# Kernel tuning notes

Hardware: AMD Instinct MI355X
Metric: run time of the kernel (lower is better)

Reference implementation:

```python
import jax, jax.numpy as jnp
import numpy as np

IN_FEATURES_LS = (32, 64, 128, 256)
OUT_FEATURES = 1024
B, T = 16, 4096


def setup_inputs() -> dict:
    key = jax.random.key(0)
    k_x, k_idx, k_w, k_b = jax.random.split(key, 4)
    n = len(IN_FEATURES_LS)
    x = jax.random.normal(k_x, (B, T, OUT_FEATURES), dtype=jnp.float32)
    # per-row declared feature size, drawn from the configured list
    branch_idx = jax.random.randint(k_idx, (B, T), 0, n)
    in_feat_size = jnp.array(IN_FEATURES_LS, dtype=jnp.int32)[branch_idx]
    # kaiming_uniform_(a=sqrt(5)) on (n, out, out): fan_in = out, bound = 1/sqrt(fan_in)
    bound_w = 1.0 / np.sqrt(OUT_FEATURES)
    weight = jax.random.uniform(k_w, (n, OUT_FEATURES, OUT_FEATURES), dtype=jnp.float32,
                                minval=-bound_w, maxval=bound_w)
    bound_b = 1.0 / np.sqrt(OUT_FEATURES)
    bias = jax.random.uniform(k_b, (n, OUT_FEATURES), dtype=jnp.float32,
                              minval=-bound_b, maxval=bound_b)
    return {"x": x, "in_feat_size": in_feat_size, "weight": weight, "bias": bias}


def reference(x, in_feat_size, weight, bias):
    # Loop over the small fixed set of feature-size branches (matches original).
    out = jnp.zeros(x.shape[:-1] + (OUT_FEATURES,), dtype=x.dtype)
    for idx, feat_size in enumerate(IN_FEATURES_LS):
        mask = (in_feat_size == feat_size)[..., None].astype(x.dtype)  # [B,T,1]
        y = jnp.einsum('oi,bti->bto', weight[idx], x) + bias[idx]
        out = out + mask * y
    return out
```

## Files before the change

### kernel.cpp

```cpp
#include <hip/hip_runtime.h>
#include <hip/hip_bf16.h>

#define OUTF 1024
#define NROWS 65536
#define NBR 4
#define BM 128
#define BN 256
#define BK 64
#define KITERS 16
#define ABYTES 16384
#define BBYTES 32768
#define BUFB 49152
#define NWG 2064

typedef __attribute__((ext_vector_type(8))) short short8;
typedef __attribute__((ext_vector_type(4))) float f32x4;

__device__ inline unsigned short f2bf(float f) {
    return __builtin_bit_cast(unsigned short, (__bf16)f);
}
__device__ inline void gload_lds16(const void* g, void* l) {
    __builtin_amdgcn_global_load_lds(
        (const __attribute__((address_space(1))) void*)g,
        (__attribute__((address_space(3))) void*)l, 16, 0, 0);
}
__device__ inline short8 pack8(float4 a, float4 b) {
    short8 o;
    o[0] = (short)f2bf(a.x); o[1] = (short)f2bf(a.y);
    o[2] = (short)f2bf(a.z); o[3] = (short)f2bf(a.w);
    o[4] = (short)f2bf(b.x); o[5] = (short)f2bf(b.y);
    o[6] = (short)f2bf(b.z); o[7] = (short)f2bf(b.w);
    return o;
}

__global__ void k_count(const int* __restrict__ feat, int* __restrict__ cnt) {
    __shared__ int lc[NBR];
    int tid = threadIdx.x;
    if (tid < NBR) lc[tid] = 0;
    __syncthreads();
    int r = blockIdx.x * 256 + tid;
    int b = 26 - __clz(feat[r]);
    atomicAdd(&lc[b], 1);
    __syncthreads();
    if (tid < NBR && lc[tid]) atomicAdd(&cnt[tid], lc[tid]);
}

__global__ void k_prefix(int* __restrict__ ws) {
    if (threadIdx.x == 0) {
        int s = 0;
        for (int b = 0; b < NBR; b++) { ws[4 + b] = s; s += ws[b]; ws[8 + b] = 0; }
    }
}

__global__ void k_fill(const int* __restrict__ feat, int* __restrict__ ws,
                       int* __restrict__ rowlist) {
    int tid = threadIdx.x;
    int lane = tid & 63;
    int r = blockIdx.x * 256 + tid;
    int b = 26 - __clz(feat[r]);
    #pragma unroll
    for (int bb = 0; bb < NBR; bb++) {
        unsigned long long mask = __ballot(b == bb);
        int leader = __ffsll((long long)mask) - 1;
        int cntw = __popcll(mask);
        int basepos = 0;
        if (lane == leader) basepos = atomicAdd(&ws[8 + bb], cntw);
        basepos = __shfl(basepos, leader < 0 ? 0 : leader);
        if (b == bb) {
            int prefix = __popcll(mask & ((1ull << lane) - 1ull));
            rowlist[ws[4 + bb] + basepos + prefix] = r;
        }
    }
}

__global__ void k_convw(const float* __restrict__ w, unsigned short* __restrict__ wsw) {
    int idx = (int)blockIdx.x * 256 + (int)threadIdx.x;
    int branch = idx >> 17;
    int rem = idx & 131071;
    int n = rem >> 7;
    int c8 = rem & 127;
    int cb = c8 << 4;
    int kw = cb >> 7;
    int wb_ = cb & 127;
    int src = kw * 64 + (((wb_) ^ ((n & 7) << 4)) >> 1);
    const float4* s = reinterpret_cast<const float4*>(
        w + ((size_t)branch << 20) + (size_t)n * OUTF + src);
    float4 v0 = s[0], v1 = s[1];
    char* dst = reinterpret_cast<char*>(wsw) + ((size_t)branch << 21) + (size_t)n * 2048 + cb;
    *reinterpret_cast<short8*>(dst) = pack8(v0, v1);
}

__global__ __launch_bounds__(512, 2)
void k_gemm4(const float* __restrict__ x,
             const unsigned short* __restrict__ wsw,
             const float* __restrict__ bias,
             const int* __restrict__ ws_i,
             const int* __restrict__ rowlist,
             float* __restrict__ out) {
    extern __shared__ char lds[];

    const int d = (int)blockIdx.x;
    const int work = (d & 7) * (NWG >> 3) + (d >> 3);
    const int mtile = work >> 2;
    const int ntile = work & 3;

    int branch = -1, lt = 0, cnt = 0, rbase = 0;
    int t_ = mtile;
    #pragma unroll
    for (int b = 0; b < NBR; b++) {
        if (branch < 0) {
            int c = ws_i[b];
            int nt = (c + 127) >> 7;
            if (t_ < nt) { branch = b; lt = t_; cnt = c; rbase = ws_i[4 + b]; }
            else t_ -= nt;
        }
    }
    if (branch < 0) return;

    const int tid = threadIdx.x;
    const int lane = tid & 63;
    const int w8 = tid >> 6;
    const int wm = (w8 >> 2) * 64;
    const int wn = (w8 & 3) * 64;
    const int n0 = ntile * BN;

    const int sarow = tid >> 2;
    const int sacol = (tid & 3) << 4;
    int aridx = rbase + lt * BM + sarow;
    int agrow = rowlist[aridx < NROWS ? aridx : 0];
    const float4* pa = reinterpret_cast<const float4*>(x + (size_t)agrow * OUTF + sacol);
    const int awb0 = sarow * 128 + (((tid & 3) * 32) ^ ((sarow & 7) << 4));
    const int awb1 = sarow * 128 + ((((tid & 3) * 32) + 16) ^ ((sarow & 7) << 4));

    const char* gb[4];
    #pragma unroll
    for (int i = 0; i < 4; i++) {
        int brow_ = i * 64 + (tid >> 3);
        gb[i] = reinterpret_cast<const char*>(wsw) + ((size_t)branch << 21)
                + (size_t)(n0 + brow_) * 2048 + ((tid & 7) << 4);
    }
    const int ldsoffB = tid * 16;

    f32x4 acc[4][4];
    #pragma unroll
    for (int i = 0; i < 4; i++)
        #pragma unroll
        for (int j = 0; j < 4; j++) acc[i][j] = (f32x4){0.f, 0.f, 0.f, 0.f};

    const int swz = (lane & 7) << 4;
    const int kq = (lane >> 4) << 4;
    const int arowb = (wm + (lane & 15)) * 128;
    const int browb = (wn + (lane & 15)) * 128;

    float4 ra[4], rn[4];

    #pragma unroll
    for (int i = 0; i < 4; i++) ra[i] = pa[i];
    #pragma unroll
    for (int i = 0; i < 4; i++)
        gload_lds16(gb[i], lds + ABYTES + i * 8192 + ldsoffB);
    *reinterpret_cast<short8*>(lds + awb0) = pack8(ra[0], ra[1]);
    *reinterpret_cast<short8*>(lds + awb1) = pack8(ra[2], ra[3]);
    #pragma unroll
    for (int i = 0; i < 4; i++) ra[i] = pa[16 + i];
    #pragma unroll
    for (int i = 0; i < 4; i++)
        gload_lds16(gb[i] + 128, lds + BUFB + ABYTES + i * 8192 + ldsoffB);
    asm volatile("s_waitcnt vmcnt(8) lgkmcnt(0)" ::: "memory");
    __builtin_amdgcn_sched_barrier(0);
    __builtin_amdgcn_s_barrier();
    __builtin_amdgcn_sched_barrier(0);

    short8 af[4], bf_[4];

    for (int t = 0; t < KITERS; ++t) {
        char* Ac = lds + (t % 3) * BUFB;
        char* Bc = Ac + ABYTES;

        if (t < KITERS - 2) {
            #pragma unroll
            for (int i = 0; i < 4; i++) rn[i] = pa[(t + 2) * 16 + i];
            char* Bn = lds + ((t + 2) % 3) * BUFB + ABYTES;
            #pragma unroll
            for (int i = 0; i < 4; i++)
                gload_lds16(gb[i] + (t + 2) * 128, Bn + i * 8192 + ldsoffB);
        }
        if (t < KITERS - 1) {
            char* An = lds + ((t + 1) % 3) * BUFB;
            *reinterpret_cast<short8*>(An + awb0) = pack8(ra[0], ra[1]);
            *reinterpret_cast<short8*>(An + awb1) = pack8(ra[2], ra[3]);
        }
        #pragma unroll
        for (int kh = 0; kh < 2; kh++) {
            const int kb = kh * 64 + kq;
            #pragma unroll
            for (int i = 0; i < 4; i++)
                af[i] = *reinterpret_cast<const short8*>(Ac + arowb + i * 2048 + (kb ^ swz));
            #pragma unroll
            for (int i = 0; i < 4; i++)
                bf_[i] = *reinterpret_cast<const short8*>(Bc + browb + i * 2048 + (kb ^ swz));
            __builtin_amdgcn_s_setprio(1);
            #pragma unroll
            for (int i = 0; i < 4; i++)
                #pragma unroll
                for (int j = 0; j < 4; j++)
                    acc[i][j] = __builtin_amdgcn_mfma_f32_16x16x32_bf16(af[i], bf_[j], acc[i][j], 0, 0, 0);
            __builtin_amdgcn_s_setprio(0);
        }
        #pragma unroll
        for (int i = 0; i < 4; i++) ra[i] = rn[i];

        if (t < KITERS - 2) {
            asm volatile("s_waitcnt vmcnt(8) lgkmcnt(0)" ::: "memory");
        } else {
            asm volatile("s_waitcnt vmcnt(0) lgkmcnt(0)" ::: "memory");
        }
        __builtin_amdgcn_sched_barrier(0);
        __builtin_amdgcn_s_barrier();
        __builtin_amdgcn_sched_barrier(0);
    }

    const int ccol = lane & 15;
    const int crow = (lane >> 4) << 2;
    float bv[4];
    const float* bp = bias + branch * OUTF + n0 + wn;
    #pragma unroll
    for (int fn = 0; fn < 4; fn++) bv[fn] = bp[fn * 16 + ccol];
    #pragma unroll
    for (int fm = 0; fm < 4; fm++) {
        #pragma unroll
        for (int j = 0; j < 4; j++) {
            int gm = lt * BM + wm + fm * 16 + crow + j;
            if (gm < cnt) {
                int orow = rowlist[rbase + gm];
                float* orp = out + (size_t)orow * OUTF + n0 + wn;
                #pragma unroll
                for (int fn = 0; fn < 4; fn++)
                    orp[fn * 16 + ccol] = acc[fm][fn][j] + bv[fn];
            }
        }
    }
}

__global__ __launch_bounds__(256, 3)
void k_gemm_fb(const float* __restrict__ x,
               const float* __restrict__ wf,
               const float* __restrict__ bias,
               const int* __restrict__ ws_i,
               const int* __restrict__ rowlist,
               float* __restrict__ out) {
    __shared__ unsigned short As[128][72];
    __shared__ unsigned short Bs[128][72];

    int t = (int)blockIdx.x;
    int branch = -1, ltile = 0, cnt = 0, rbase = 0;
    #pragma unroll
    for (int b = 0; b < NBR; b++) {
        if (branch < 0) {
            int c = ws_i[b];
            int nt = (c + 127) >> 7;
            if (t < nt) { branch = b; ltile = t; cnt = c; rbase = ws_i[4 + b]; }
            else t -= nt;
        }
    }
    if (branch < 0) return;

    const int tid = threadIdx.x;
    const int lane = tid & 63;
    const int wid = tid >> 6;
    const int wm = (wid & 1) << 6;
    const int wn = (wid >> 1) << 6;
    const int n0 = (int)blockIdx.y * 128;

    const int srow = tid >> 1;
    const int scol = (tid & 1) << 5;

    const int gmrow = ltile * 128 + srow;
    const int grow = (gmrow < cnt) ? rowlist[rbase + gmrow] : -1;
    const float* xsrc = x + (size_t)(grow < 0 ? 0 : grow) * OUTF + scol;
    const float* wfsrc = wf + ((size_t)branch << 20) + (size_t)(n0 + srow) * OUTF + scol;

    f32x4 acc[4][4];
    #pragma unroll
    for (int i = 0; i < 4; i++)
        #pragma unroll
        for (int j = 0; j < 4; j++)
            acc[i][j] = (f32x4){0.f, 0.f, 0.f, 0.f};

    for (int k0 = 0; k0 < OUTF; k0 += 64) {
        {
            unsigned short* dst = &As[srow][scol];
            if (grow >= 0) {
                const float4* s4 = reinterpret_cast<const float4*>(xsrc + k0);
                #pragma unroll
                for (int i = 0; i < 8; i++) {
                    float4 v = s4[i];
                    ushort4 o;
                    o.x = f2bf(v.x); o.y = f2bf(v.y); o.z = f2bf(v.z); o.w = f2bf(v.w);
                    reinterpret_cast<ushort4*>(dst)[i] = o;
                }
            } else {
                ushort4 z; z.x = z.y = z.z = z.w = 0;
                #pragma unroll
                for (int i = 0; i < 8; i++) reinterpret_cast<ushort4*>(dst)[i] = z;
            }
        }
        {
            unsigned short* dst = &Bs[srow][scol];
            const float4* s4 = reinterpret_cast<const float4*>(wfsrc + k0);
            #pragma unroll
            for (int i = 0; i < 8; i++) {
                float4 v = s4[i];
                ushort4 o;
                o.x = f2bf(v.x); o.y = f2bf(v.y); o.z = f2bf(v.z); o.w = f2bf(v.w);
                reinterpret_cast<ushort4*>(dst)[i] = o;
            }
        }
        __syncthreads();
        #pragma unroll
        for (int kk = 0; kk < 64; kk += 32) {
            const int krd = kk + (lane >> 4) * 8;
            short8 af[4], bf_[4];
            #pragma unroll
            for (int i = 0; i < 4; i++)
                af[i] = *reinterpret_cast<const short8*>(&As[wm + i * 16 + (lane & 15)][krd]);
            #pragma unroll
            for (int i = 0; i < 4; i++)
                bf_[i] = *reinterpret_cast<const short8*>(&Bs[wn + i * 16 + (lane & 15)][krd]);
            #pragma unroll
            for (int i = 0; i < 4; i++)
                #pragma unroll
                for (int j = 0; j < 4; j++)
                    acc[i][j] = __builtin_amdgcn_mfma_f32_16x16x32_bf16(af[i], bf_[j], acc[i][j], 0, 0, 0);
        }
        __syncthreads();
    }

    const int ccol = lane & 15;
    const int crow = (lane >> 4) << 2;
    float bv[4];
    const float* bp = bias + branch * OUTF + n0 + wn;
    #pragma unroll
    for (int fn = 0; fn < 4; fn++) bv[fn] = bp[fn * 16 + ccol];
    #pragma unroll
    for (int fm = 0; fm < 4; fm++) {
        #pragma unroll
        for (int j = 0; j < 4; j++) {
            int gm = ltile * 128 + wm + fm * 16 + crow + j;
            if (gm < cnt) {
                int orow = rowlist[rbase + gm];
                float* orp = out + (size_t)orow * OUTF + n0 + wn;
                #pragma unroll
                for (int fn = 0; fn < 4; fn++)
                    orp[fn * 16 + ccol] = acc[fm][fn][j] + bv[fn];
            }
        }
    }
}

extern "C" void kernel_launch(void* const* d_in, const int* in_sizes, int n_in,
                              void* d_out, int out_size, void* d_ws, size_t ws_size,
                              hipStream_t stream) {
    const float* x = (const float*)d_in[0];
    const int* feat = (const int*)d_in[1];
    const float* w = (const float*)d_in[2];
    const float* bias = (const float*)d_in[3];
    float* out = (float*)d_out;

    char* ws = (char*)d_ws;
    int* ws_i = (int*)ws;
    int* rowlist = (int*)(ws + 256);
    const size_t WB_OFF = (size_t)512 << 10;
    unsigned short* wsw = (unsigned short*)(ws + WB_OFF);
    const size_t need = WB_OFF + (size_t)NBR * OUTF * OUTF * 2;

    (void)hipMemsetAsync(ws_i, 0, 64, stream);
    k_count<<<NROWS / 256, 256, 0, stream>>>(feat, ws_i);
    k_prefix<<<1, 64, 0, stream>>>(ws_i);
    k_fill<<<NROWS / 256, 256, 0, stream>>>(feat, ws_i, rowlist);

    if (ws_size >= need) {
        k_convw<<<2048, 256, 0, stream>>>(w, wsw);
        (void)hipFuncSetAttribute((const void*)k_gemm4,
                                  hipFuncAttributeMaxDynamicSharedMemorySize, 3 * BUFB);
        k_gemm4<<<NWG, 512, 3 * BUFB, stream>>>(x, wsw, bias, ws_i, rowlist, out);
    } else {
        dim3 grid(NROWS / 128 + NBR, OUTF / 128);
        k_gemm_fb<<<grid, 256, 0, stream>>>(x, w, bias, ws_i, rowlist, out);
    }
}
```

Baseline: 358.9 us.

## Pre-gather x into swizzled bf16 buffer and enlarge GEMM M-tile to 256

Adds a k_convx pass that gathers rows of x by branch into a padded, pre-swizzled bf16 workspace buffer. The GEMM can then stream both A and B straight into LDS with global_load_lds, instead of loading fp32 into registers and converting inside the main loop. The GEMM tile grows to 256x256, with 8x4 accumulators per wave, a triple-buffered A and double-buffered B, and 160KB of LDS. Branch segment offsets are padded to multiples of 256 so each tile stays within one branch. The cost is an extra full read/write pass over x and lower occupancy, since the LDS footprint limits the CU to one block.

```diff
diff --git a/kernel.cpp b/kernel.cpp
--- a/kernel.cpp
+++ b/kernel.cpp
@@ -4,14 +4,8 @@
 #define OUTF 1024
 #define NROWS 65536
 #define NBR 4
-#define BM 128
-#define BN 256
-#define BK 64
-#define KITERS 16
-#define ABYTES 16384
-#define BBYTES 32768
-#define BUFB 49152
-#define NWG 2064
+#define XBROWS 66560
+#define NWG 1040
 
 typedef __attribute__((ext_vector_type(8))) short short8;
 typedef __attribute__((ext_vector_type(4))) float f32x4;
@@ -48,7 +42,11 @@
 __global__ void k_prefix(int* __restrict__ ws) {
     if (threadIdx.x == 0) {
         int s = 0;
-        for (int b = 0; b < NBR; b++) { ws[4 + b] = s; s += ws[b]; ws[8 + b] = 0; }
+        for (int b = 0; b < NBR; b++) {
+            ws[4 + b] = s;
+            s = (s + ws[b] + 255) & ~255;
+            ws[8 + b] = 0;
+        }
     }
 }
 
@@ -78,20 +76,33 @@
     int branch = idx >> 17;
     int rem = idx & 131071;
     int n = rem >> 7;
-    int c8 = rem & 127;
-    int cb = c8 << 4;
+    int cb = (rem & 127) << 4;
     int kw = cb >> 7;
     int wb_ = cb & 127;
-    int src = kw * 64 + (((wb_) ^ ((n & 7) << 4)) >> 1);
+    int src = kw * 64 + ((wb_ ^ ((n & 7) << 4)) >> 1);
     const float4* s = reinterpret_cast<const float4*>(
         w + ((size_t)branch << 20) + (size_t)n * OUTF + src);
-    float4 v0 = s[0], v1 = s[1];
     char* dst = reinterpret_cast<char*>(wsw) + ((size_t)branch << 21) + (size_t)n * 2048 + cb;
-    *reinterpret_cast<short8*>(dst) = pack8(v0, v1);
+    *reinterpret_cast<short8*>(dst) = pack8(s[0], s[1]);
+}
+
+__global__ void k_convx(const float* __restrict__ x, const int* __restrict__ rowlist,
+                        unsigned short* __restrict__ xb) {
+    int g = (int)blockIdx.x * 512 + (int)threadIdx.x;
+    int orow = g >> 7;
+    int cb = (g & 127) << 4;
+    int rl = rowlist[orow];
+    if ((unsigned)rl >= NROWS) rl = 0;
+    int kw = cb >> 7;
+    int wb_ = cb & 127;
+    int src = kw * 64 + ((wb_ ^ ((orow & 7) << 4)) >> 1);
+    const float4* s = reinterpret_cast<const float4*>(x + (size_t)rl * OUTF + src);
+    char* dst = reinterpret_cast<char*>(xb) + (size_t)orow * 2048 + cb;
+    *reinterpret_cast<short8*>(dst) = pack8(s[0], s[1]);
 }
 
 __global__ __launch_bounds__(512, 2)
-void k_gemm4(const float* __restrict__ x,
+void k_gemm5(const unsigned short* __restrict__ xb,
              const unsigned short* __restrict__ wsw,
              const float* __restrict__ bias,
              const int* __restrict__ ws_i,
@@ -110,7 +121,7 @@
     for (int b = 0; b < NBR; b++) {
         if (branch < 0) {
             int c = ws_i[b];
-            int nt = (c + 127) >> 7;
+            int nt = (c + 255) >> 8;
             if (t_ < nt) { branch = b; lt = t_; cnt = c; rbase = ws_i[4 + b]; }
             else t_ -= nt;
         }
@@ -120,30 +131,25 @@
     const int tid = threadIdx.x;
     const int lane = tid & 63;
     const int w8 = tid >> 6;
-    const int wm = (w8 >> 2) * 64;
+    const int wm = (w8 >> 2) * 128;
     const int wn = (w8 & 3) * 64;
-    const int n0 = ntile * BN;
-
-    const int sarow = tid >> 2;
-    const int sacol = (tid & 3) << 4;
-    int aridx = rbase + lt * BM + sarow;
-    int agrow = rowlist[aridx < NROWS ? aridx : 0];
-    const float4* pa = reinterpret_cast<const float4*>(x + (size_t)agrow * OUTF + sacol);
-    const int awb0 = sarow * 128 + (((tid & 3) * 32) ^ ((sarow & 7) << 4));
-    const int awb1 = sarow * 128 + ((((tid & 3) * 32) + 16) ^ ((sarow & 7) << 4));
-
-    const char* gb[4];
+    const int n0 = ntile * 256;
+    const int row0 = rbase + lt * 256;
+
+    const char* gA[4];
+    const char* gB[4];
     #pragma unroll
     for (int i = 0; i < 4; i++) {
-        int brow_ = i * 64 + (tid >> 3);
-        gb[i] = reinterpret_cast<const char*>(wsw) + ((size_t)branch << 21)
-                + (size_t)(n0 + brow_) * 2048 + ((tid & 7) << 4);
-    }
-    const int ldsoffB = tid * 16;
-
-    f32x4 acc[4][4];
-    #pragma unroll
-    for (int i = 0; i < 4; i++)
+        int r = i * 64 + (tid >> 3);
+        gA[i] = reinterpret_cast<const char*>(xb) + (size_t)(row0 + r) * 2048 + ((tid & 7) << 4);
+        gB[i] = reinterpret_cast<const char*>(wsw) + ((size_t)branch << 21)
+                + (size_t)(n0 + r) * 2048 + ((tid & 7) << 4);
+    }
+    const int ldsoff = tid << 4;
+
+    f32x4 acc[8][4];
+    #pragma unroll
+    for (int i = 0; i < 8; i++)
         #pragma unroll
         for (int j = 0; j < 4; j++) acc[i][j] = (f32x4){0.f, 0.f, 0.f, 0.f};
 
@@ -152,72 +158,63 @@
     const int arowb = (wm + (lane & 15)) * 128;
     const int browb = (wn + (lane & 15)) * 128;
 
-    float4 ra[4], rn[4];
-
-    #pragma unroll
-    for (int i = 0; i < 4; i++) ra[i] = pa[i];
-    #pragma unroll
-    for (int i = 0; i < 4; i++)
-        gload_lds16(gb[i], lds + ABYTES + i * 8192 + ldsoffB);
-    *reinterpret_cast<short8*>(lds + awb0) = pack8(ra[0], ra[1]);
-    *reinterpret_cast<short8*>(lds + awb1) = pack8(ra[2], ra[3]);
-    #pragma unroll
-    for (int i = 0; i < 4; i++) ra[i] = pa[16 + i];
-    #pragma unroll
-    for (int i = 0; i < 4; i++)
-        gload_lds16(gb[i] + 128, lds + BUFB + ABYTES + i * 8192 + ldsoffB);
-    asm volatile("s_waitcnt vmcnt(8) lgkmcnt(0)" ::: "memory");
+    #pragma unroll
+    for (int i = 0; i < 4; i++) gload_lds16(gA[i], lds + i * 8192 + ldsoff);
+    #pragma unroll
+    for (int i = 0; i < 4; i++) gload_lds16(gA[i] + 128, lds + 32768 + i * 8192 + ldsoff);
+    #pragma unroll
+    for (int i = 0; i < 4; i++) gload_lds16(gB[i], lds + 98304 + i * 8192 + ldsoff);
+    asm volatile("s_waitcnt vmcnt(0)" ::: "memory");
     __builtin_amdgcn_sched_barrier(0);
     __builtin_amdgcn_s_barrier();
     __builtin_amdgcn_sched_barrier(0);
 
-    short8 af[4], bf_[4];
-
-    for (int t = 0; t < KITERS; ++t) {
-        char* Ac = lds + (t % 3) * BUFB;
-        char* Bc = Ac + ABYTES;
-
-        if (t < KITERS - 2) {
-            #pragma unroll
-            for (int i = 0; i < 4; i++) rn[i] = pa[(t + 2) * 16 + i];
-            char* Bn = lds + ((t + 2) % 3) * BUFB + ABYTES;
-            #pragma unroll
-            for (int i = 0; i < 4; i++)
-                gload_lds16(gb[i] + (t + 2) * 128, Bn + i * 8192 + ldsoffB);
-        }
-        if (t < KITERS - 1) {
-            char* An = lds + ((t + 1) % 3) * BUFB;
-            *reinterpret_cast<short8*>(An + awb0) = pack8(ra[0], ra[1]);
-            *reinterpret_cast<short8*>(An + awb1) = pack8(ra[2], ra[3]);
-        }
-        #pragma unroll
-        for (int kh = 0; kh < 2; kh++) {
-            const int kb = kh * 64 + kq;
-            #pragma unroll
-            for (int i = 0; i < 4; i++)
+    int ia = 0;
+    for (int t = 0; t < 16; ++t) {
+        char* Ac = lds + ia * 32768;
+        char* Bc = lds + 98304 + (t & 1) * 32768;
+
+        if (t < 15) {
+            char* Bn = lds + 98304 + ((t + 1) & 1) * 32768;
+            #pragma unroll
+            for (int i = 0; i < 4; i++)
+                gload_lds16(gB[i] + (t + 1) * 128, Bn + i * 8192 + ldsoff);
+        }
+        if (t < 14) {
+            int ia2 = ia + 2; if (ia2 >= 3) ia2 -= 3;
+            char* An = lds + ia2 * 32768;
+            #pragma unroll
+            for (int i = 0; i < 4; i++)
+                gload_lds16(gA[i] + (t + 2) * 128, An + i * 8192 + ldsoff);
+        }
+        __builtin_amdgcn_sched_barrier(0);
+
+        __builtin_amdgcn_s_setprio(1);
+        #pragma unroll
+        for (int ks = 0; ks < 2; ks++) {
+            const int kb = (ks << 6) + kq;
+            short8 af[8], bf_[4];
+            #pragma unroll
+            for (int i = 0; i < 8; i++)
                 af[i] = *reinterpret_cast<const short8*>(Ac + arowb + i * 2048 + (kb ^ swz));
             #pragma unroll
-            for (int i = 0; i < 4; i++)
-                bf_[i] = *reinterpret_cast<const short8*>(Bc + browb + i * 2048 + (kb ^ swz));
-            __builtin_amdgcn_s_setprio(1);
-            #pragma unroll
-            for (int i = 0; i < 4; i++)
+            for (int j = 0; j < 4; j++)
+                bf_[j] = *reinterpret_cast<const short8*>(Bc + browb + j * 2048 + (kb ^ swz));
+            #pragma unroll
+            for (int i = 0; i < 8; i++)
                 #pragma unroll
                 for (int j = 0; j < 4; j++)
                     acc[i][j] = __builtin_amdgcn_mfma_f32_16x16x32_bf16(af[i], bf_[j], acc[i][j], 0, 0, 0);
-            __builtin_amdgcn_s_setprio(0);
-        }
-        #pragma unroll
-        for (int i = 0; i < 4; i++) ra[i] = rn[i];
-
-        if (t < KITERS - 2) {
-            asm volatile("s_waitcnt vmcnt(8) lgkmcnt(0)" ::: "memory");
-        } else {
-            asm volatile("s_waitcnt vmcnt(0) lgkmcnt(0)" ::: "memory");
-        }
+        }
+        __builtin_amdgcn_s_setprio(0);
+
+        if (t < 14) { asm volatile("s_waitcnt vmcnt(4)" ::: "memory"); }
+        else        { asm volatile("s_waitcnt vmcnt(0)" ::: "memory"); }
         __builtin_amdgcn_sched_barrier(0);
         __builtin_amdgcn_s_barrier();
         __builtin_amdgcn_sched_barrier(0);
+
+        ia = (ia + 1 == 3) ? 0 : ia + 1;
     }
 
     const int ccol = lane & 15;
@@ -227,10 +224,10 @@
     #pragma unroll
     for (int fn = 0; fn < 4; fn++) bv[fn] = bp[fn * 16 + ccol];
     #pragma unroll
-    for (int fm = 0; fm < 4; fm++) {
+    for (int fm = 0; fm < 8; fm++) {
         #pragma unroll
         for (int j = 0; j < 4; j++) {
-            int gm = lt * BM + wm + fm * 16 + crow + j;
+            int gm = lt * 256 + wm + fm * 16 + crow + j;
             if (gm < cnt) {
                 int orow = rowlist[rbase + gm];
                 float* orp = out + (size_t)orow * OUTF + n0 + wn;
@@ -293,27 +290,23 @@
             if (grow >= 0) {
                 const float4* s4 = reinterpret_cast<const float4*>(xsrc + k0);
                 #pragma unroll
-                for (int i = 0; i < 8; i++) {
-                    float4 v = s4[i];
-                    ushort4 o;
-                    o.x = f2bf(v.x); o.y = f2bf(v.y); o.z = f2bf(v.z); o.w = f2bf(v.w);
-                    reinterpret_cast<ushort4*>(dst)[i] = o;
+                for (int i = 0; i < 8; i += 2) {
+                    float4 v0 = s4[i], v1 = s4[i + 1];
+                    *reinterpret_cast<short8*>(dst + i * 4) = pack8(v0, v1);
                 }
             } else {
-                ushort4 z; z.x = z.y = z.z = z.w = 0;
-                #pragma unroll
-                for (int i = 0; i < 8; i++) reinterpret_cast<ushort4*>(dst)[i] = z;
+                short8 z = (short8){0,0,0,0,0,0,0,0};
+                #pragma unroll
+                for (int i = 0; i < 8; i += 2) *reinterpret_cast<short8*>(dst + i * 4) = z;
             }
         }
         {
             unsigned short* dst = &Bs[srow][scol];
             const float4* s4 = reinterpret_cast<const float4*>(wfsrc + k0);
             #pragma unroll
-            for (int i = 0; i < 8; i++) {
-                float4 v = s4[i];
-                ushort4 o;
-                o.x = f2bf(v.x); o.y = f2bf(v.y); o.z = f2bf(v.z); o.w = f2bf(v.w);
-                reinterpret_cast<ushort4*>(dst)[i] = o;
+            for (int i = 0; i < 8; i += 2) {
+                float4 v0 = s4[i], v1 = s4[i + 1];
+                *reinterpret_cast<short8*>(dst + i * 4) = pack8(v0, v1);
             }
         }
         __syncthreads();
@@ -370,20 +363,23 @@
     char* ws = (char*)d_ws;
     int* ws_i = (int*)ws;
     int* rowlist = (int*)(ws + 256);
-    const size_t WB_OFF = (size_t)512 << 10;
-    unsigned short* wsw = (unsigned short*)(ws + WB_OFF);
-    const size_t need = WB_OFF + (size_t)NBR * OUTF * OUTF * 2;
+    const size_t WSW_OFF = (size_t)512 << 10;
+    const size_t XB_OFF = (size_t)9 << 20;
+    unsigned short* wsw = (unsigned short*)(ws + WSW_OFF);
+    unsigned short* xb = (unsigned short*)(ws + XB_OFF);
+    const size_t need_full = XB_OFF + (size_t)XBROWS * 2048;
 
     (void)hipMemsetAsync(ws_i, 0, 64, stream);
     k_count<<<NROWS / 256, 256, 0, stream>>>(feat, ws_i);
     k_prefix<<<1, 64, 0, stream>>>(ws_i);
     k_fill<<<NROWS / 256, 256, 0, stream>>>(feat, ws_i, rowlist);
 
-    if (ws_size >= need) {
+    if (ws_size >= need_full) {
         k_convw<<<2048, 256, 0, stream>>>(w, wsw);
-        (void)hipFuncSetAttribute((const void*)k_gemm4,
-                                  hipFuncAttributeMaxDynamicSharedMemorySize, 3 * BUFB);
-        k_gemm4<<<NWG, 512, 3 * BUFB, stream>>>(x, wsw, bias, ws_i, rowlist, out);
+        k_convx<<<(XBROWS * 128) / 512, 512, 0, stream>>>(x, rowlist, xb);
+        (void)hipFuncSetAttribute((const void*)k_gemm5,
+                                  hipFuncAttributeMaxDynamicSharedMemorySize, 163840);
+        k_gemm5<<<NWG, 512, 163840, stream>>>(xb, wsw, bias, ws_i, rowlist, out);
     } else {
         dim3 grid(NROWS / 128 + NBR, OUTF / 128);
         k_gemm_fb<<<grid, 256, 0, stream>>>(x, w, bias, ws_i, rowlist, out);
```

New measurement: 352.3 us. No clear change (-1.8%).
